# Kernel optimization log

Measured on AMD Instinct MI355X. Metric: run time of the kernel, lower is better.

## Reference

```python
import jax, jax.numpy as jnp
import numpy as np

B, XDIM, TWIN, INCH = 1024, 62, 10, 128
MID, OUT, K, K1, LIN, HC = 256, 512, 3, 10, 512, 4
EPS = 1e-5

REGIONS = [
    list(range(0, 5)),
    list(range(5, 8)) + list(range(14, 17)),
    list(range(8, 11)) + list(range(17, 20)),
    list(range(11, 14)) + list(range(20, 23)),
    list(range(23, 26)) + list(range(32, 35)),
    list(range(26, 29)) + list(range(35, 38)),
    list(range(29, 32)) + list(range(38, 41)),
    list(range(41, 44)) + list(range(50, 52)) + list(range(57, 58)),
    list(range(44, 47)) + list(range(52, 55)) + list(range(58, 61)),
    list(range(47, 50)) + list(range(55, 57)) + list(range(61, 62)),
]


def setup_inputs() -> dict:
    key = jax.random.key(0)
    ks = jax.random.split(key, 40)
    n = lambda k, s, sc=0.02: jax.random.normal(k, s, jnp.float32) * sc
    inp = {
        "x": jax.random.normal(ks[0], (B, XDIM, TWIN, INCH), jnp.float32),
        "tfe_w": n(ks[1], (XDIM, TWIN)),          # depthwise Conv2d (10,1) weight, squeezed
        "tfe_b": jnp.zeros((XDIM,), jnp.float32),
        "cheby1_w": n(ks[2], (K, INCH, OUT)),
        "A": n(ks[3], (XDIM, XDIM)),
        "cheby2_w": n(ks[4], (K, MID, OUT)),
        "A1": n(ks[5], (K1, K1)),
        "b_gate": jnp.float32(1.0),
        "c_gate": jnp.float32(1.0),
        "region_b": jnp.zeros((K1, MID), jnp.float32),
        "hc_w1": n(ks[6], (OUT * 72, LIN)),
        "hc_b1": jnp.zeros((LIN,), jnp.float32),
        "bn1_g": jnp.ones((LIN,), jnp.float32),
        "bn1_b": jnp.zeros((LIN,), jnp.float32),
        "hc_w2": n(ks[7], (LIN, LIN // 2)),
        "hc_b2": jnp.zeros((LIN // 2,), jnp.float32),
        "bn2_g": jnp.ones((LIN // 2,), jnp.float32),
        "bn2_b": jnp.zeros((LIN // 2,), jnp.float32),
        "hc_w3": n(ks[8], (LIN // 2, HC)),
        "hc_b3": jnp.zeros((HC,), jnp.float32),
    }
    for i, idx in enumerate(REGIONS):
        inp[f"rw{i+1}"] = n(ks[10 + i], (MID, INCH, len(idx)))
    return inp


def _cheby(x, L, Ws):
    # sum_k  S_k @ x @ W_k  with S_0 = I, S_k = S_{k-1} @ L ; then ReLU
    S = jnp.eye(L.shape[0], dtype=x.dtype)
    res = jnp.zeros(x.shape[:2] + (Ws.shape[-1],), x.dtype)
    for k in range(Ws.shape[0]):
        res = res + jnp.einsum("nm,bmt,to->bno", S, x, Ws[k])
        S = S @ L
    return jax.nn.relu(res)


def _bn(h, g, b):
    mu = h.mean(axis=0)
    v = h.var(axis=0)  # biased, training-mode BatchNorm1d
    return (h - mu) * jax.lax.rsqrt(v + EPS) * g + b


def _forward(x, tfe_w, tfe_b, cheby1_w, A, cheby2_w, A1, b_gate, c_gate,
             rw1, rw2, rw3, rw4, rw5, rw6, rw7, rw8, rw9, rw10, region_b,
             hc_w1, hc_b1, bn1_g, bn1_b, hc_w2, hc_b2, bn2_g, bn2_b, hc_w3, hc_b3):
    # variance gate (torch.var default: unbiased)
    sigma = jnp.var(x, axis=2, ddof=1)                              # (B, 62, INCH)
    g_tfe = jnp.einsum("bcit,ci->bct", x, tfe_w) + tfe_b[None, :, None]
    g = g_tfe * jnp.exp(-sigma)                                      # (B, 62, INCH)

    g1 = _cheby(g, A, cheby1_w)                                      # (B, 62, OUT)

    rws = [rw1, rw2, rw3, rw4, rw5, rw6, rw7, rw8, rw9, rw10]
    RG = []
    for i, (idx, w) in enumerate(zip(REGIONS, rws)):
        reg = g[:, jnp.asarray(idx), :]                              # (B, L, INCH)
        RG.append(jnp.einsum("blc,mcl->bm", reg, w) + region_b[i])   # Conv1d, full-width kernel
    g2in = jnp.stack(RG, axis=1)                                     # (B, 10, MID)
    g2 = _cheby(g2in, A1, cheby2_w)                                  # (B, 10, OUT)

    att = jnp.concatenate([b_gate * g1, c_gate * g2], axis=1)        # (B, 72, OUT)
    cat = jnp.concatenate([g1, g2], axis=1)
    out = jax.nn.softmax(att, axis=1) * cat
    out = out.reshape(out.shape[0], -1)                              # (B, 72*OUT)

    h = jax.nn.gelu(_bn(out @ hc_w1 + hc_b1, bn1_g, bn1_b), approximate=False)
    h = jax.nn.gelu(_bn(h @ hc_w2 + hc_b2, bn2_g, bn2_b), approximate=False)
    h = h @ hc_w3 + hc_b3
    return jax.nn.softmax(h, axis=1)


def reference(x, tfe_w, tfe_b, cheby1_w, A, cheby2_w, A1, b_gate, c_gate,
              rw1, rw2, rw3, rw4, rw5, rw6, rw7, rw8, rw9, rw10, region_b,
              hc_w1, hc_b1, bn1_g, bn1_b, hc_w2, hc_b2, bn2_g, bn2_b, hc_w3, hc_b3):
    return _forward(x, tfe_w, tfe_b, cheby1_w, A, cheby2_w, A1, b_gate, c_gate,
                    rw1, rw2, rw3, rw4, rw5, rw6, rw7, rw8, rw9, rw10, region_b,
                    hc_w1, hc_b1, bn1_g, bn1_b, hc_w2, hc_b2, bn2_g, bn2_b, hc_w3, hc_b3)
```

## Files before the change

### kernel.cpp

```cpp
#include <hip/hip_runtime.h>
#include <math.h>


__constant__ int cOrder[62] = {
  0,1,2,3,4,
  5,6,7,14,15,16,
  8,9,10,17,18,19,
  11,12,13,20,21,22,
  23,24,25,32,33,34,
  26,27,28,35,36,37,
  29,30,31,38,39,40,
  41,42,43,50,51,57,
  44,45,46,52,53,54,58,59,60,
  47,48,49,55,56,61
};
__constant__ int cPos[62] = {
  0,1,2,3,4, 5,6,7, 11,12,13, 17,18,19, 8,9,10, 14,15,16, 20,21,22,
  23,24,25, 29,30,31, 35,36,37, 26,27,28, 32,33,34, 38,39,40,
  41,42,43, 47,48,49, 56,57,58, 44,45, 50,51,52, 59,60, 46, 53,54,55, 61
};
__constant__ int cRegK[10]   = {640,768,768,768,768,768,768,768,1152,768};
__constant__ int cRegCum[10] = {0,640,1408,2176,2944,3712,4480,5248,6016,7168};

struct Ptr10 { const float* p[10]; };

typedef __attribute__((ext_vector_type(8))) short bf16x8;
typedef __attribute__((ext_vector_type(4))) float f32x4;

__device__ __forceinline__ float gelu_exact(float v){
  return 0.5f * v * (1.0f + erff(v * 0.70710678118654752f));
}
__device__ __forceinline__ unsigned short f2bf(float f){
  unsigned u = __float_as_uint(f);
  unsigned r = (u + 0x7fffu + ((u >> 16) & 1u)) >> 16;
  return (unsigned short)r;
}
__device__ __forceinline__ float bf2f(unsigned short u){
  return __uint_as_float(((unsigned)u) << 16);
}
__device__ __forceinline__ void load_lds16(const unsigned short* g, unsigned short* l){
  __builtin_amdgcn_global_load_lds(
      (const __attribute__((address_space(1))) void*)g,
      (__attribute__((address_space(3))) void*)l, 16, 0, 0);
}

template<bool RELU>
__global__ __launch_bounds__(256) void k_mfma(
    const unsigned short* __restrict__ A, long lda,
    const unsigned short* __restrict__ BT, long ldb,
    void* __restrict__ Cv, int ldc, int kPerZ, long cStrideZ, int mcCount){
  __shared__ unsigned short As[128*32];
  __shared__ unsigned short Bs[128*32];
  int mt, nt, zt;
  if (mcCount){
    int id = blockIdx.x;
    int c = ((id >> 6) << 3) + (id & 7);
    int member = (id >> 3) & 7;
    zt = c / mcCount;
    int mc = c - zt*mcCount;
    mt = mc*2 + (member >> 2);
    nt = member & 3;
  } else { mt = blockIdx.x; nt = blockIdx.y; zt = blockIdx.z; }
  int tid = threadIdx.x;
  int wave = tid >> 6, lane = tid & 63;
  int m0 = mt * 128, n0 = nt * 128;
  int kStart = zt * kPerZ;
  int waveM = wave >> 1, waveN = wave & 1;
  int lr = lane >> 2, ch = lane & 3;
  int quad = lane >> 4, mrow = lane & 15;
  int swe = ((quad ^ (mrow & 3)) << 3);

  int rA0 = wave*32 + lr;
  int rA1 = rA0 + 16;
  int ce  = ((ch ^ (rA0 & 3)) << 3);
  const unsigned short* gA0 = A  + (long)(m0 + rA0)*lda + kStart + ce;
  const unsigned short* gA1 = A  + (long)(m0 + rA1)*lda + kStart + ce;
  const unsigned short* gB0 = BT + (long)(n0 + rA0)*ldb + kStart + ce;
  const unsigned short* gB1 = BT + (long)(n0 + rA1)*ldb + kStart + ce;
  unsigned short* lA0 = &As[(wave*32)*32];
  unsigned short* lA1 = &As[(wave*32+16)*32];
  unsigned short* lB0 = &Bs[(wave*32)*32];
  unsigned short* lB1 = &Bs[(wave*32+16)*32];

  f32x4 acc[4][4] = {};
  int nIter = kPerZ >> 5;
  for (int it = 0; it < nIter; ++it){
    long ko = (long)it << 5;
    load_lds16(gA0 + ko, lA0);
    load_lds16(gA1 + ko, lA1);
    load_lds16(gB0 + ko, lB0);
    load_lds16(gB1 + ko, lB1);
    __syncthreads();
    bf16x8 af[4], bfr[4];
#pragma unroll
    for (int mi = 0; mi < 4; mi++)
      af[mi] = *(const bf16x8*)&As[(waveM*64 + mi*16 + mrow)*32 + swe];
#pragma unroll
    for (int ni = 0; ni < 4; ni++)
      bfr[ni] = *(const bf16x8*)&Bs[(waveN*64 + ni*16 + mrow)*32 + swe];
#pragma unroll
    for (int mi = 0; mi < 4; mi++)
#pragma unroll
      for (int ni = 0; ni < 4; ni++)
        acc[mi][ni] = __builtin_amdgcn_mfma_f32_16x16x32_bf16(
            af[mi], bfr[ni], acc[mi][ni], 0, 0, 0);
    __syncthreads();
  }
  if (RELU){
    unsigned short* C = (unsigned short*)Cv;
#pragma unroll
    for (int mi = 0; mi < 4; mi++)
#pragma unroll
      for (int ni = 0; ni < 4; ni++){
        int col = n0 + waveN*64 + ni*16 + mrow;
#pragma unroll
        for (int r = 0; r < 4; r++){
          int row = m0 + waveM*64 + mi*16 + quad*4 + r;
          C[(long)row*ldc + col] = f2bf(fmaxf(acc[mi][ni][r], 0.f));
        }
      }
  } else {
    float* C = (float*)Cv + (long)zt * cStrideZ;
#pragma unroll
    for (int mi = 0; mi < 4; mi++)
#pragma unroll
      for (int ni = 0; ni < 4; ni++){
        int col = n0 + waveN*64 + ni*16 + mrow;
#pragma unroll
        for (int r = 0; r < 4; r++){
          int row = m0 + waveM*64 + mi*16 + quad*4 + r;
          C[(long)row*ldc + col] = acc[mi][ni][r];
        }
      }
  }
}
template __global__ void k_mfma<true>(const unsigned short*, long, const unsigned short*, long, void*, int, int, long, int);
template __global__ void k_mfma<false>(const unsigned short*, long, const unsigned short*, long, void*, int, int, long, int);

__global__ __launch_bounds__(256) void k_dual(
    const unsigned short* __restrict__ A2c, const unsigned short* __restrict__ B2c,
    unsigned short* __restrict__ C2c,
    const unsigned short* __restrict__ A1c, const unsigned short* __restrict__ B1c,
    unsigned short* __restrict__ C1c){
  __shared__ unsigned short As[128*32];
  __shared__ unsigned short Bs[128*32];
  int id = blockIdx.x;
  bool is1 = id >= 320;
  const unsigned short* A  = is1 ? A1c : A2c;
  const unsigned short* BT = is1 ? B1c : B2c;
  unsigned short* C = is1 ? C1c : C2c;
  long lda = is1 ? 384 : 768;
  long ldb = lda;
  int kPerZ = (int)lda;
  if (is1) id -= 320;
  int c = ((id >> 6) << 3) + (id & 7);
  int member = (id >> 3) & 7;
  int mt = c*2 + (member >> 2);
  int nt = member & 3;
  int tid = threadIdx.x;
  int wave = tid >> 6, lane = tid & 63;
  int m0 = mt * 128, n0 = nt * 128;
  int waveM = wave >> 1, waveN = wave & 1;
  int lr = lane >> 2, ch = lane & 3;
  int quad = lane >> 4, mrow = lane & 15;
  int swe = ((quad ^ (mrow & 3)) << 3);

  int rA0 = wave*32 + lr;
  int rA1 = rA0 + 16;
  int ce  = ((ch ^ (rA0 & 3)) << 3);
  const unsigned short* gA0 = A  + (long)(m0 + rA0)*lda + ce;
  const unsigned short* gA1 = A  + (long)(m0 + rA1)*lda + ce;
  const unsigned short* gB0 = BT + (long)(n0 + rA0)*ldb + ce;
  const unsigned short* gB1 = BT + (long)(n0 + rA1)*ldb + ce;
  unsigned short* lA0 = &As[(wave*32)*32];
  unsigned short* lA1 = &As[(wave*32+16)*32];
  unsigned short* lB0 = &Bs[(wave*32)*32];
  unsigned short* lB1 = &Bs[(wave*32+16)*32];

  f32x4 acc[4][4] = {};
  int nIter = kPerZ >> 5;
  for (int it = 0; it < nIter; ++it){
    long ko = (long)it << 5;
    load_lds16(gA0 + ko, lA0);
    load_lds16(gA1 + ko, lA1);
    load_lds16(gB0 + ko, lB0);
    load_lds16(gB1 + ko, lB1);
    __syncthreads();
    bf16x8 af[4], bfr[4];
#pragma unroll
    for (int mi = 0; mi < 4; mi++)
      af[mi] = *(const bf16x8*)&As[(waveM*64 + mi*16 + mrow)*32 + swe];
#pragma unroll
    for (int ni = 0; ni < 4; ni++)
      bfr[ni] = *(const bf16x8*)&Bs[(waveN*64 + ni*16 + mrow)*32 + swe];
#pragma unroll
    for (int mi = 0; mi < 4; mi++)
#pragma unroll
      for (int ni = 0; ni < 4; ni++)
        acc[mi][ni] = __builtin_amdgcn_mfma_f32_16x16x32_bf16(
            af[mi], bfr[ni], acc[mi][ni], 0, 0, 0);
    __syncthreads();
  }
#pragma unroll
  for (int mi = 0; mi < 4; mi++)
#pragma unroll
    for (int ni = 0; ni < 4; ni++){
      int col = n0 + waveN*64 + ni*16 + mrow;
#pragma unroll
      for (int r = 0; r < 4; r++){
        int row = m0 + waveM*64 + mi*16 + quad*4 + r;
        C[(long)row*512 + col] = f2bf(fmaxf(acc[mi][ni][r], 0.f));
      }
    }
}

__global__ __launch_bounds__(256) void k_mid(
    const unsigned short* __restrict__ ARb, const unsigned short* __restrict__ Ab,
    const unsigned short* __restrict__ A2b, unsigned short* __restrict__ xcat,
    const unsigned short* __restrict__ RWT, const float* __restrict__ regb,
    float* __restrict__ g2in){
  __shared__ __align__(16) char smraw[32768];
  int id = blockIdx.x;
  int tid = threadIdx.x;
  if (id < 1024){
    unsigned short* gT  = (unsigned short*)smraw;
    unsigned short* AbL = gT + 128*64;
    int b = id;
    const unsigned short* arp = ARb + (long)b*7936;
    for (int i = tid; i < 7936; i += 256){
      int p = i >> 7, c = i & 127;
      int m = cOrder[p];
      gT[(c<<6) + (((m>>3) ^ (c&7))<<3) + (m&7)] = arp[i];
    }
    {
      int c = tid >> 1, m = 62 + (tid & 1);
      gT[(c<<6) + ((7 ^ (c&7))<<3) + (m&7)] = 0;
    }
    for (int q = tid; q < 1024; q += 256){
      int mm = q >> 9, qq = q & 511;
      int row = qq >> 3, ch = qq & 7;
      const unsigned short* src = mm ? A2b : Ab;
      *(bf16x8*)&AbL[mm*4096 + (row<<6) + ((ch ^ (row&7))<<3)] =
        *(const bf16x8*)&src[(row<<6) + (ch<<3)];
    }
    __syncthreads();
    int wave = tid >> 6, lane = tid & 63;
    int quad = lane >> 4, mrow = lane & 15;
    int mat = wave >> 1, wc = wave & 1;
    const unsigned short* Am = AbL + mat*4096;
    f32x4 acc[4][4] = {};
#pragma unroll
    for (int s = 0; s < 2; s++){
      bf16x8 af[4], bfr[4];
#pragma unroll
      for (int mi = 0; mi < 4; mi++){
        int row = mi*16 + mrow;
        af[mi] = *(const bf16x8*)&Am[(row<<6) + ((((s<<2)|quad) ^ (row&7))<<3)];
      }
#pragma unroll
      for (int ni = 0; ni < 4; ni++){
        int row = wc*64 + ni*16 + mrow;
        bfr[ni] = *(const bf16x8*)&gT[(row<<6) + ((((s<<2)|quad) ^ (row&7))<<3)];
      }
#pragma unroll
      for (int mi = 0; mi < 4; mi++)
#pragma unroll
        for (int ni = 0; ni < 4; ni++)
          acc[mi][ni] = __builtin_amdgcn_mfma_f32_16x16x32_bf16(
              af[mi], bfr[ni], acc[mi][ni], 0, 0, 0);
    }
    long xb = (long)b*23808 + (mat+1)*128;
#pragma unroll
    for (int mi = 0; mi < 4; mi++)
#pragma unroll
      for (int ni = 0; ni < 4; ni++){
        int c = wc*64 + ni*16 + mrow;
#pragma unroll
        for (int r = 0; r < 4; r++){
          int n = mi*16 + quad*4 + r;
          if (n < 62) xcat[xb + (long)n*384 + c] = f2bf(acc[mi][ni][r]);
        }
      }
    return;
  }
  unsigned short* As = (unsigned short*)smraw;
  unsigned short* Bs = As + 128*32;
  int id2 = id - 1024;
  int z = id2 >> 4;
  int m  = id2 & 15;
  int mt = m >> 1, nt = m & 1;
  int K = cRegK[z];
  int cumk = cRegCum[z];
  const unsigned short* A  = ARb + cumk;
  const unsigned short* BT = RWT + (long)cumk*256;
  long lda = 7936, ldb = K;
  int wave = tid >> 6, lane = tid & 63;
  int m0 = mt * 128, n0 = nt * 128;
  int waveM = wave >> 1, waveN = wave & 1;
  int lr = lane >> 2, ch = lane & 3;
  int quad = lane >> 4, mrow = lane & 15;
  int swe = ((quad ^ (mrow & 3)) << 3);

  int rA0 = wave*32 + lr;
  int rA1 = rA0 + 16;
  int ce  = ((ch ^ (rA0 & 3)) << 3);
  const unsigned short* gA0 = A  + (long)(m0 + rA0)*lda + ce;
  const unsigned short* gA1 = A  + (long)(m0 + rA1)*lda + ce;
  const unsigned short* gB0 = BT + (long)(n0 + rA0)*ldb + ce;
  const unsigned short* gB1 = BT + (long)(n0 + rA1)*ldb + ce;
  unsigned short* lA0 = &As[(wave*32)*32];
  unsigned short* lA1 = &As[(wave*32+16)*32];
  unsigned short* lB0 = &Bs[(wave*32)*32];
  unsigned short* lB1 = &Bs[(wave*32+16)*32];

  f32x4 acc[4][4] = {};
  int nIter = K >> 5;
  for (int it = 0; it < nIter; ++it){
    long ko = (long)it << 5;
    load_lds16(gA0 + ko, lA0);
    load_lds16(gA1 + ko, lA1);
    load_lds16(gB0 + ko, lB0);
    load_lds16(gB1 + ko, lB1);
    __syncthreads();
    bf16x8 af[4], bfr[4];
#pragma unroll
    for (int mi = 0; mi < 4; mi++)
      af[mi] = *(const bf16x8*)&As[(waveM*64 + mi*16 + mrow)*32 + swe];
#pragma unroll
    for (int ni = 0; ni < 4; ni++)
      bfr[ni] = *(const bf16x8*)&Bs[(waveN*64 + ni*16 + mrow)*32 + swe];
#pragma unroll
    for (int mi = 0; mi < 4; mi++)
#pragma unroll
      for (int ni = 0; ni < 4; ni++)
        acc[mi][ni] = __builtin_amdgcn_mfma_f32_16x16x32_bf16(
            af[mi], bfr[ni], acc[mi][ni], 0, 0, 0);
    __syncthreads();
  }
#pragma unroll
  for (int mi = 0; mi < 4; mi++)
#pragma unroll
    for (int ni = 0; ni < 4; ni++){
      int col = n0 + waveN*64 + ni*16 + mrow;
      float bias = regb[z*256 + col];
#pragma unroll
      for (int r = 0; r < 4; r++){
        int row = m0 + waveM*64 + mi*16 + quad*4 + r;
        g2in[(long)row*2560 + z*256 + col] = acc[mi][ni][r] + bias;
      }
    }
}

__global__ __launch_bounds__(256) void k_front(
    const float* __restrict__ s0, unsigned short* __restrict__ d0,
    const float* __restrict__ s1, unsigned short* __restrict__ d1,
    const float* __restrict__ s2, unsigned short* __restrict__ d2,
    const float* __restrict__ s3, unsigned short* __restrict__ d3,
    Ptr10 rws, unsigned short* __restrict__ RWT,
    const float* __restrict__ Amat, unsigned short* __restrict__ AbW,
    unsigned short* __restrict__ A2bW,
    const float* __restrict__ x, const float* __restrict__ tw,
    const float* __restrict__ tb, unsigned short* __restrict__ arb,
    unsigned short* __restrict__ xcat, float* __restrict__ sumz){
  __shared__ float smem[64*65];
  int id = blockIdx.x;
  int tid = threadIdx.x;
  if (id >= 15342){
    *(float4*)(sumz + (id-15342)*1024 + tid*4) = make_float4(0.f,0.f,0.f,0.f);
    return;
  }
  if (id >= 7406){
    int q = id - 7406;
    int r = tid >> 5, j = tid & 31;
    int idx = q*8 + r;
    int b = idx / 62, n = idx - b*62;
    const float4* xp = (const float4*)(x + (long)idx*1280) + j;
    float sx=0.f,sy=0.f,sz=0.f,sw=0.f;
    float qx=0.f,qy=0.f,qz=0.f,qw=0.f;
    float gx=0.f,gy=0.f,gz=0.f,gw=0.f;
#pragma unroll
    for (int i = 0; i < 10; i++){
      float4 v = xp[i*32];
      float w = tw[n*10+i];
      sx+=v.x; sy+=v.y; sz+=v.z; sw+=v.w;
      qx=fmaf(v.x,v.x,qx); qy=fmaf(v.y,v.y,qy);
      qz=fmaf(v.z,v.z,qz); qw=fmaf(v.w,v.w,qw);
      gx=fmaf(v.x,w,gx); gy=fmaf(v.y,w,gy);
      gz=fmaf(v.z,w,gz); gw=fmaf(v.w,w,gw);
    }
    float tbn = tb[n];
    float mx_=sx*0.1f, my_=sy*0.1f, mz_=sz*0.1f, mw_=sw*0.1f;
    float rx = (gx+tbn)*expf(-(qx-10.f*mx_*mx_)*(1.f/9.f));
    float ry = (gy+tbn)*expf(-(qy-10.f*my_*my_)*(1.f/9.f));
    float rz = (gz+tbn)*expf(-(qz-10.f*mz_*mz_)*(1.f/9.f));
    float rw = (gw+tbn)*expf(-(qw-10.f*mw_*mw_)*(1.f/9.f));
    ushort4 u = make_ushort4(f2bf(rx), f2bf(ry), f2bf(rz), f2bf(rw));
    *(ushort4*)(arb  + (long)b*7936  + cPos[n]*128 + j*4) = u;
    *(ushort4*)(xcat + (long)b*23808 + n*384       + j*4) = u;
    return;
  }
  if (id < 7344 && id >= 4784){
    int q = id - 4784;
    int z = q >> 8, m = q & 255;
    int K = cRegK[z], L = K >> 7;
    const float* rw = rws.p[z] + (long)m*K;
    unsigned short* dst = RWT + (long)cRegCum[z]*256 + (long)m*K;
    for (int i = tid; i < K; i += 256) smem[i] = rw[i];
    __syncthreads();
    for (int k = tid; k < K; k += 256){
      int l = k >> 7, c = k & 127;
      dst[k] = f2bf(smem[c*L + l]);
    }
    return;
  }
  if (id >= 7344){
    int r = id - 7344, c = tid;
    if (c < 62) smem[c] = Amat[r*62 + c];
    __syncthreads();
    if (c < 64){
      unsigned short av = 0, a2v = 0;
      if (c < 62){
        av = f2bf(smem[c]);
        float s = 0.f;
        for (int t = 0; t < 62; t++) s = fmaf(smem[t], Amat[t*62 + c], s);
        a2v = f2bf(s);
      }
      AbW [r*64 + c] = av;
      A2bW[r*64 + c] = a2v;
    }
    if (r == 0 && c >= 64 && c < 192){
      int q = c - 64;
      int rr = 62 + (q >> 6), cc = q & 63;
      AbW [rr*64 + cc] = 0;
      A2bW[rr*64 + cc] = 0;
    }
    return;
  }
  const float* src; unsigned short* dst; int R, C, rt, ct;
  if (id < 4608){ src=s0; dst=d0; R=36864; C=512; rt=id>>3;  ct=id&7; }
  else if (id < 4640){ int q=id-4608; src=s1; dst=d1; R=512; C=256; rt=q>>2; ct=q&3; }
  else if (id < 4688){ int q=id-4640; src=s2; dst=d2; R=384; C=512; rt=q>>3; ct=q&7; }
  else { int q=id-4688; src=s3; dst=d3; R=768; C=512; rt=q>>3; ct=q&7; }
  int r0 = rt*64, c0 = ct*64;
  int rr = tid >> 2, cb = (tid & 3) << 2;
#pragma unroll
  for (int i = 0; i < 4; i++){
    int cc = cb + i*16;
    float4 v = *(const float4*)(src + (long)(r0+rr)*C + c0 + cc);
    smem[rr*65+cc+0]=v.x; smem[rr*65+cc+1]=v.y;
    smem[rr*65+cc+2]=v.z; smem[rr*65+cc+3]=v.w;
  }
  __syncthreads();
  int cc = tid >> 2, rb = (tid & 3) << 2;
#pragma unroll
  for (int i = 0; i < 4; i++){
    int r = rb + i*16;
    ushort4 u = make_ushort4(f2bf(smem[(r+0)*65+cc]), f2bf(smem[(r+1)*65+cc]),
                             f2bf(smem[(r+2)*65+cc]), f2bf(smem[(r+3)*65+cc]));
    *(ushort4*)(dst + (long)(c0+cc)*R + r0 + r) = u;
  }
}

__global__ __launch_bounds__(256) void k_x2cat(
    const float* __restrict__ g2in, const float* __restrict__ A1,
    unsigned short* __restrict__ X2){
  __shared__ float sg[2560];
  __shared__ float sA1[100];
  __shared__ float sA2[100];
  int b = blockIdx.x, tid = threadIdx.x;
  for (int i = tid; i < 2560; i += 256) sg[i] = g2in[(long)b*2560 + i];
  if (tid < 100) sA1[tid] = A1[tid];
  __syncthreads();
  if (tid < 100){
    int n = tid/10, m = tid - n*10;
    float a = 0.f;
#pragma unroll
    for (int t = 0; t < 10; t++) a = fmaf(sA1[n*10+t], sA1[t*10+m], a);
    sA2[tid] = a;
  }
  __syncthreads();
  for (int i = tid; i < 2560; i += 256){
    int n = i >> 8, t = i & 255;
    float v1 = 0.f, v2 = 0.f;
#pragma unroll
    for (int m = 0; m < 10; m++){
      float gv = sg[(m<<8) + t];
      v1 = fmaf(sA1[n*10+m], gv, v1);
      v2 = fmaf(sA2[n*10+m], gv, v2);
    }
    long base = (long)b*7680 + n*768;
    X2[base + t]       = f2bf(sg[i]);
    X2[base + 256 + t] = f2bf(v1);
    X2[base + 512 + t] = f2bf(v2);
  }
}

__global__ __launch_bounds__(256) void k_softcat(
    const unsigned short* __restrict__ g1, const unsigned short* __restrict__ g2,
    const float* __restrict__ bg_, const float* __restrict__ cg_,
    unsigned short* __restrict__ outb){
  int b = blockIdx.x;
  int o = blockIdx.y*256 + threadIdx.x;
  float v[72];
  const unsigned short* p1 = g1 + (long)b*62*512 + o;
#pragma unroll
  for (int j = 0; j < 62; j++) v[j] = bf2f(p1[j*512]);
  const unsigned short* p2 = g2 + (long)b*10*512 + o;
#pragma unroll
  for (int j = 0; j < 10; j++) v[62+j] = bf2f(p2[j*512]);
  float bg = *bg_, cg = *cg_;
  float mx = -1e30f;
#pragma unroll
  for (int j = 0; j < 72; j++){
    float av = (j < 62 ? bg : cg) * v[j];
    mx = fmaxf(mx, av);
  }
  float sum = 0.f;
#pragma unroll
  for (int j = 0; j < 72; j++){
    float e = expf((j < 62 ? bg : cg) * v[j] - mx);
    sum += e;
    v[j] = e * v[j];
  }
  float inv = 1.f / sum;
  unsigned short* op = outb + (long)b*36864 + o;
#pragma unroll
  for (int j = 0; j < 72; j++) op[j*512] = f2bf(v[j] * inv);
}

__global__ __launch_bounds__(256) void k_tail1(
    const float4* __restrict__ P, const float* __restrict__ gam,
    const float* __restrict__ bet, float* __restrict__ sum,
    float* __restrict__ ssq, unsigned int* __restrict__ cnt,
    unsigned short* __restrict__ h1b){
  __shared__ float4 ls[128], ls2[128];
  int tid = threadIdx.x;
  int c  = tid & 127;
  int rr = tid >> 7;
  int r0 = blockIdx.x * 8;
  float4 va[4];
  float4 s1 = make_float4(0.f,0.f,0.f,0.f);
  float4 s2 = make_float4(0.f,0.f,0.f,0.f);
#pragma unroll
  for (int k = 0; k < 4; k++){
    int row = r0 + rr + 2*k;
    long idx = (long)row*128 + c;
    float4 v = make_float4(0.f,0.f,0.f,0.f);
#pragma unroll
    for (int s = 0; s < 16; s++){
      float4 p = P[(long)s*131072 + idx];
      v.x += p.x; v.y += p.y; v.z += p.z; v.w += p.w;
    }
    va[k] = v;
    s1.x += v.x; s1.y += v.y; s1.z += v.z; s1.w += v.w;
    s2.x = fmaf(v.x,v.x,s2.x); s2.y = fmaf(v.y,v.y,s2.y);
    s2.z = fmaf(v.z,v.z,s2.z); s2.w = fmaf(v.w,v.w,s2.w);
  }
  if (rr){ ls[c] = s1; ls2[c] = s2; }
  __syncthreads();
  if (!rr){
    float4 o1 = ls[c], o2 = ls2[c];
    atomicAdd(&sum[c*4+0], s1.x+o1.x); atomicAdd(&sum[c*4+1], s1.y+o1.y);
    atomicAdd(&sum[c*4+2], s1.z+o1.z); atomicAdd(&sum[c*4+3], s1.w+o1.w);
    atomicAdd(&ssq[c*4+0], s2.x+o2.x); atomicAdd(&ssq[c*4+1], s2.y+o2.y);
    atomicAdd(&ssq[c*4+2], s2.z+o2.z); atomicAdd(&ssq[c*4+3], s2.w+o2.w);
  }
  __threadfence();
  __syncthreads();
  if (tid == 0){
    __hip_atomic_fetch_add(cnt, 1u, __ATOMIC_RELEASE, __HIP_MEMORY_SCOPE_AGENT);
    while (__hip_atomic_load(cnt, __ATOMIC_ACQUIRE, __HIP_MEMORY_SCOPE_AGENT) < 128u)
      __builtin_amdgcn_s_sleep(16);
  }
  __syncthreads();
  int j = c*4;
  float mu0 = __hip_atomic_load(&sum[j+0], __ATOMIC_RELAXED, __HIP_MEMORY_SCOPE_AGENT)*(1.f/1024.f);
  float mu1 = __hip_atomic_load(&sum[j+1], __ATOMIC_RELAXED, __HIP_MEMORY_SCOPE_AGENT)*(1.f/1024.f);
  float mu2 = __hip_atomic_load(&sum[j+2], __ATOMIC_RELAXED, __HIP_MEMORY_SCOPE_AGENT)*(1.f/1024.f);
  float mu3 = __hip_atomic_load(&sum[j+3], __ATOMIC_RELAXED, __HIP_MEMORY_SCOPE_AGENT)*(1.f/1024.f);
  float q0 = __hip_atomic_load(&ssq[j+0], __ATOMIC_RELAXED, __HIP_MEMORY_SCOPE_AGENT);
  float q1 = __hip_atomic_load(&ssq[j+1], __ATOMIC_RELAXED, __HIP_MEMORY_SCOPE_AGENT);
  float q2 = __hip_atomic_load(&ssq[j+2], __ATOMIC_RELAXED, __HIP_MEMORY_SCOPE_AGENT);
  float q3 = __hip_atomic_load(&ssq[j+3], __ATOMIC_RELAXED, __HIP_MEMORY_SCOPE_AGENT);
  float rs0 = rsqrtf(q0*(1.f/1024.f) - mu0*mu0 + 1e-5f);
  float rs1 = rsqrtf(q1*(1.f/1024.f) - mu1*mu1 + 1e-5f);
  float rs2 = rsqrtf(q2*(1.f/1024.f) - mu2*mu2 + 1e-5f);
  float rs3 = rsqrtf(q3*(1.f/1024.f) - mu3*mu3 + 1e-5f);
  float g0 = gam[j+0], g1 = gam[j+1], g2 = gam[j+2], g3 = gam[j+3];
  float b0 = bet[j+0], b1 = bet[j+1], b2 = bet[j+2], b3 = bet[j+3];
#pragma unroll
  for (int k = 0; k < 4; k++){
    int row = r0 + rr + 2*k;
    float4 v = va[k];
    ushort4 u;
    u.x = f2bf(gelu_exact((v.x - mu0)*rs0*g0 + b0));
    u.y = f2bf(gelu_exact((v.y - mu1)*rs1*g1 + b1));
    u.z = f2bf(gelu_exact((v.z - mu2)*rs2*g2 + b2));
    u.w = f2bf(gelu_exact((v.w - mu3)*rs3*g3 + b3));
    *(ushort4*)(h1b + (long)row*512 + j) = u;
  }
}

__global__ __launch_bounds__(256) void k_tail2(
    const float* __restrict__ P2, const float* __restrict__ gam,
    const float* __restrict__ bet, const float* __restrict__ w3,
    const float* __restrict__ b3, float* __restrict__ sum,
    float* __restrict__ ssq, unsigned int* __restrict__ cnt,
    float* __restrict__ outp){
  __shared__ float lv[32][257];
  __shared__ float rd[32][8][4];
  int tid = threadIdx.x;
  int rbase = blockIdx.x * 32;
  float v[32];
  float s = 0.f, s2 = 0.f;
#pragma unroll 8
  for (int r = 0; r < 32; r++){
    int row = rbase + r;
    float a = 0.f;
#pragma unroll
    for (int sp = 0; sp < 4; sp++)
      a += P2[((long)sp*1024 + row)*256 + tid];
    v[r] = a;
    s += a; s2 = fmaf(a, a, s2);
  }
  atomicAdd(&sum[tid], s);
  atomicAdd(&ssq[tid], s2);
  __threadfence();
  __syncthreads();
  if (tid == 0){
    __hip_atomic_fetch_add(cnt, 1u, __ATOMIC_RELEASE, __HIP_MEMORY_SCOPE_AGENT);
    while (__hip_atomic_load(cnt, __ATOMIC_ACQUIRE, __HIP_MEMORY_SCOPE_AGENT) < 32u)
      __builtin_amdgcn_s_sleep(16);
  }
  __syncthreads();
  float mu = __hip_atomic_load(&sum[tid], __ATOMIC_RELAXED, __HIP_MEMORY_SCOPE_AGENT)*(1.f/1024.f);
  float qq = __hip_atomic_load(&ssq[tid], __ATOMIC_RELAXED, __HIP_MEMORY_SCOPE_AGENT);
  float rs = rsqrtf(qq*(1.f/1024.f) - mu*mu + 1e-5f);
  float gm = gam[tid], bt = bet[tid];
#pragma unroll 8
  for (int r = 0; r < 32; r++)
    lv[r][tid] = gelu_exact((v[r] - mu)*rs*gm + bt);
  __syncthreads();
  int row = tid >> 3, seg = tid & 7;
  float p0=0.f,p1=0.f,p2=0.f,p3=0.f;
#pragma unroll
  for (int i = 0; i < 32; i++){
    int cc = seg*32 + i;
    float a = lv[row][cc];
    float4 w = ((const float4*)w3)[cc];
    p0 = fmaf(a, w.x, p0); p1 = fmaf(a, w.y, p1);
    p2 = fmaf(a, w.z, p2); p3 = fmaf(a, w.w, p3);
  }
  rd[row][seg][0]=p0; rd[row][seg][1]=p1; rd[row][seg][2]=p2; rd[row][seg][3]=p3;
  __syncthreads();
  if (tid < 32){
    float l[4];
#pragma unroll
    for (int c = 0; c < 4; c++){
      float a = 0.f;
#pragma unroll
      for (int g = 0; g < 8; g++) a += rd[tid][g][c];
      l[c] = a + b3[c];
    }
    float m = fmaxf(fmaxf(l[0], l[1]), fmaxf(l[2], l[3]));
    float e[4]; float su = 0.f;
#pragma unroll
    for (int c = 0; c < 4; c++){ e[c] = expf(l[c]-m); su += e[c]; }
    float inv = 1.f / su;
#pragma unroll
    for (int c = 0; c < 4; c++) outp[(long)(rbase+tid)*4 + c] = e[c]*inv;
  }
}

extern "C" void kernel_launch(void* const* d_in, const int* in_sizes, int n_in,
                              void* d_out, int out_size, void* d_ws, size_t ws_size,
                              hipStream_t stream){
  (void)n_in; (void)out_size; (void)ws_size;
  bool dictOrder = (in_sizes[9] == 2560);
  const float* x     = (const float*)d_in[0];
  const float* tfe_w = (const float*)d_in[1];
  const float* tfe_b = (const float*)d_in[2];
  const float* ch1w  = (const float*)d_in[3];
  const float* Amat  = (const float*)d_in[4];
  const float* ch2w  = (const float*)d_in[5];
  const float* A1mat = (const float*)d_in[6];
  const float* bgate = (const float*)d_in[7];
  const float* cgate = (const float*)d_in[8];
  const float* regb  = (const float*)d_in[dictOrder ? 9 : 19];
  int o = dictOrder ? 0 : 10;
  const float* hc_w1 = (const float*)d_in[10+o];
  const float* bn1g  = (const float*)d_in[12+o];
  const float* bn1b  = (const float*)d_in[13+o];
  const float* hc_w2 = (const float*)d_in[14+o];
  const float* bn2g  = (const float*)d_in[16+o];
  const float* bn2b  = (const float*)d_in[17+o];
  const float* hc_w3 = (const float*)d_in[18+o];
  const float* hc_b3 = (const float*)d_in[19+o];
  Ptr10 rws;
  for (int i = 0; i < 10; i++) rws.p[i] = (const float*)d_in[(dictOrder ? 20 : 9) + i];

  char* Wb = (char*)d_ws;
  unsigned short* ARb   = (unsigned short*)(Wb + 0);
  unsigned short* XCAT  = (unsigned short*)(Wb + 16252928);
  unsigned short* RWT   = (unsigned short*)(Wb + 65011712);
  float*          G2IN  = (float*)(Wb + 69074944);
  unsigned short* X2CAT = (unsigned short*)(Wb + 79560704);
  unsigned short* W1T   = (unsigned short*)(Wb + 95289344);
  unsigned short* WC1T  = (unsigned short*)(Wb + 133038080);
  unsigned short* WC2T  = (unsigned short*)(Wb + 133431296);
  unsigned short* G1    = (unsigned short*)(Wb + 134217728);
  unsigned short* G2    = (unsigned short*)(Wb + 199229440);
  unsigned short* OUTB  = (unsigned short*)(Wb + 0);
  float*          P     = (float*)(Wb + 209715200);
  float*          SUM1  = (float*)(Wb + 246415360);
  float*          SSQ1  = SUM1 + 512;
  float*          SUM2  = SUM1 + 1024;
  float*          SSQ2  = SUM1 + 1280;
  unsigned int*   CNT1  = (unsigned int*)(SUM1 + 1536);
  unsigned int*   CNT2  = (unsigned int*)(SUM1 + 1537);
  unsigned short* Ab    = (unsigned short*)(Wb + 246423552);
  unsigned short* A2b   = (unsigned short*)(Wb + 246439040);
  unsigned short* W2T   = (unsigned short*)(Wb + 246454528);
  unsigned short* H1B   = (unsigned short*)(Wb + 246716928);

  k_front<<<15344, 256, 0, stream>>>(hc_w1, W1T, hc_w2, W2T, ch1w, WC1T,
                                     ch2w, WC2T, rws, RWT, Amat, Ab, A2b,
                                     x, tfe_w, tfe_b, ARb, XCAT, SUM1);
  k_mid<<<1184, 256, 0, stream>>>(ARb, Ab, A2b, XCAT, RWT, regb, G2IN);
  k_x2cat<<<1024, 256, 0, stream>>>(G2IN, A1mat, X2CAT);
  k_dual<<<2304, 256, 0, stream>>>(X2CAT, WC2T, G2, XCAT, WC1T, G1);
  k_softcat<<<dim3(1024,2), 256, 0, stream>>>(G1, G2, bgate, cgate, OUTB);
  k_mfma<false><<<512, 256, 0, stream>>>(OUTB, 36864, W1T, 36864, (void*)P, 512, 2304, 524288, 4);
  k_tail1<<<128, 256, 0, stream>>>((const float4*)P, bn1g, bn1b, SUM1, SSQ1, CNT1, H1B);
  k_mfma<false><<<dim3(8,2,4), 256, 0, stream>>>(H1B, 512, W2T, 512, (void*)P, 256, 128, 262144, 0);
  k_tail2<<<32, 256, 0, stream>>>(P, bn2g, bn2b, hc_w3, hc_b3, SUM2, SSQ2, CNT2, (float*)d_out);
}
```

Measured before the change: 811.9 us.

## Fuse BN1/GELU, second GEMM and BN2/head tail into one persistent kernel

Merges k_tail1, the small second MFMA GEMM and k_tail2 into a single 128-block kernel. Grid-wide counter barriers separate the stages, and later stages run on a subset of blocks. This removes two kernel launches and their gaps at the end of the pipeline. In exchange it relies on all blocks being co-resident and on four barrier counters being zeroed beforehand. The GEMM is also re-implemented inline with a single-buffered K loop.

```diff
diff --git a/kernel.cpp b/kernel.cpp
--- a/kernel.cpp
+++ b/kernel.cpp
@@ -42,6 +42,16 @@
   __builtin_amdgcn_global_load_lds(
       (const __attribute__((address_space(1))) void*)g,
       (__attribute__((address_space(3))) void*)l, 16, 0, 0);
+}
+__device__ __forceinline__ void gate(unsigned int* cnt, unsigned int target, int tid){
+  __threadfence();
+  __syncthreads();
+  if (tid == 0){
+    __hip_atomic_fetch_add(cnt, 1u, __ATOMIC_RELEASE, __HIP_MEMORY_SCOPE_AGENT);
+    while (__hip_atomic_load(cnt, __ATOMIC_ACQUIRE, __HIP_MEMORY_SCOPE_AGENT) < target)
+      __builtin_amdgcn_s_sleep(16);
+  }
+  __syncthreads();
 }
 
 template<bool RELU>
@@ -528,147 +538,191 @@
   for (int j = 0; j < 72; j++) op[j*512] = f2bf(v[j] * inv);
 }
 
-__global__ __launch_bounds__(256) void k_tail1(
-    const float4* __restrict__ P, const float* __restrict__ gam,
-    const float* __restrict__ bet, float* __restrict__ sum,
-    float* __restrict__ ssq, unsigned int* __restrict__ cnt,
-    unsigned short* __restrict__ h1b){
-  __shared__ float4 ls[128], ls2[128];
+__global__ __launch_bounds__(256) void k_tail(
+    float* Pf, const float* __restrict__ gam1, const float* __restrict__ bet1,
+    const unsigned short* __restrict__ W2T,
+    const float* __restrict__ gam2, const float* __restrict__ bet2,
+    const float* __restrict__ w3, const float* __restrict__ b3,
+    float* __restrict__ sum1, float* __restrict__ ssq1,
+    float* __restrict__ sum2, float* __restrict__ ssq2,
+    unsigned int* __restrict__ cnts, unsigned short* __restrict__ h1b,
+    float* __restrict__ outp){
+  __shared__ __align__(16) char smraw[36992];
   int tid = threadIdx.x;
-  int c  = tid & 127;
-  int rr = tid >> 7;
-  int r0 = blockIdx.x * 8;
-  float4 va[4];
-  float4 s1 = make_float4(0.f,0.f,0.f,0.f);
-  float4 s2 = make_float4(0.f,0.f,0.f,0.f);
-#pragma unroll
-  for (int k = 0; k < 4; k++){
-    int row = r0 + rr + 2*k;
-    long idx = (long)row*128 + c;
-    float4 v = make_float4(0.f,0.f,0.f,0.f);
-#pragma unroll
-    for (int s = 0; s < 16; s++){
-      float4 p = P[(long)s*131072 + idx];
-      v.x += p.x; v.y += p.y; v.z += p.z; v.w += p.w;
-    }
-    va[k] = v;
-    s1.x += v.x; s1.y += v.y; s1.z += v.z; s1.w += v.w;
-    s2.x = fmaf(v.x,v.x,s2.x); s2.y = fmaf(v.y,v.y,s2.y);
-    s2.z = fmaf(v.z,v.z,s2.z); s2.w = fmaf(v.w,v.w,s2.w);
-  }
-  if (rr){ ls[c] = s1; ls2[c] = s2; }
-  __syncthreads();
-  if (!rr){
-    float4 o1 = ls[c], o2 = ls2[c];
-    atomicAdd(&sum[c*4+0], s1.x+o1.x); atomicAdd(&sum[c*4+1], s1.y+o1.y);
-    atomicAdd(&sum[c*4+2], s1.z+o1.z); atomicAdd(&sum[c*4+3], s1.w+o1.w);
-    atomicAdd(&ssq[c*4+0], s2.x+o2.x); atomicAdd(&ssq[c*4+1], s2.y+o2.y);
-    atomicAdd(&ssq[c*4+2], s2.z+o2.z); atomicAdd(&ssq[c*4+3], s2.w+o2.w);
-  }
-  __threadfence();
-  __syncthreads();
-  if (tid == 0){
-    __hip_atomic_fetch_add(cnt, 1u, __ATOMIC_RELEASE, __HIP_MEMORY_SCOPE_AGENT);
-    while (__hip_atomic_load(cnt, __ATOMIC_ACQUIRE, __HIP_MEMORY_SCOPE_AGENT) < 128u)
-      __builtin_amdgcn_s_sleep(16);
-  }
-  __syncthreads();
-  int j = c*4;
-  float mu0 = __hip_atomic_load(&sum[j+0], __ATOMIC_RELAXED, __HIP_MEMORY_SCOPE_AGENT)*(1.f/1024.f);
-  float mu1 = __hip_atomic_load(&sum[j+1], __ATOMIC_RELAXED, __HIP_MEMORY_SCOPE_AGENT)*(1.f/1024.f);
-  float mu2 = __hip_atomic_load(&sum[j+2], __ATOMIC_RELAXED, __HIP_MEMORY_SCOPE_AGENT)*(1.f/1024.f);
-  float mu3 = __hip_atomic_load(&sum[j+3], __ATOMIC_RELAXED, __HIP_MEMORY_SCOPE_AGENT)*(1.f/1024.f);
-  float q0 = __hip_atomic_load(&ssq[j+0], __ATOMIC_RELAXED, __HIP_MEMORY_SCOPE_AGENT);
-  float q1 = __hip_atomic_load(&ssq[j+1], __ATOMIC_RELAXED, __HIP_MEMORY_SCOPE_AGENT);
-  float q2 = __hip_atomic_load(&ssq[j+2], __ATOMIC_RELAXED, __HIP_MEMORY_SCOPE_AGENT);
-  float q3 = __hip_atomic_load(&ssq[j+3], __ATOMIC_RELAXED, __HIP_MEMORY_SCOPE_AGENT);
-  float rs0 = rsqrtf(q0*(1.f/1024.f) - mu0*mu0 + 1e-5f);
-  float rs1 = rsqrtf(q1*(1.f/1024.f) - mu1*mu1 + 1e-5f);
-  float rs2 = rsqrtf(q2*(1.f/1024.f) - mu2*mu2 + 1e-5f);
-  float rs3 = rsqrtf(q3*(1.f/1024.f) - mu3*mu3 + 1e-5f);
-  float g0 = gam[j+0], g1 = gam[j+1], g2 = gam[j+2], g3 = gam[j+3];
-  float b0 = bet[j+0], b1 = bet[j+1], b2 = bet[j+2], b3 = bet[j+3];
-#pragma unroll
-  for (int k = 0; k < 4; k++){
-    int row = r0 + rr + 2*k;
-    float4 v = va[k];
-    ushort4 u;
-    u.x = f2bf(gelu_exact((v.x - mu0)*rs0*g0 + b0));
-    u.y = f2bf(gelu_exact((v.y - mu1)*rs1*g1 + b1));
-    u.z = f2bf(gelu_exact((v.z - mu2)*rs2*g2 + b2));
-    u.w = f2bf(gelu_exact((v.w - mu3)*rs3*g3 + b3));
-    *(ushort4*)(h1b + (long)row*512 + j) = u;
-  }
-}
-
-__global__ __launch_bounds__(256) void k_tail2(
-    const float* __restrict__ P2, const float* __restrict__ gam,
-    const float* __restrict__ bet, const float* __restrict__ w3,
-    const float* __restrict__ b3, float* __restrict__ sum,
-    float* __restrict__ ssq, unsigned int* __restrict__ cnt,
-    float* __restrict__ outp){
-  __shared__ float lv[32][257];
-  __shared__ float rd[32][8][4];
-  int tid = threadIdx.x;
-  int rbase = blockIdx.x * 32;
-  float v[32];
-  float s = 0.f, s2 = 0.f;
+  int bid = blockIdx.x;
+  {
+    const float4* P = (const float4*)Pf;
+    float4* ls  = (float4*)smraw;
+    float4* ls2 = ls + 128;
+    int c  = tid & 127;
+    int rr = tid >> 7;
+    int r0 = bid * 8;
+    float4 va[4];
+    float4 s1 = make_float4(0.f,0.f,0.f,0.f);
+    float4 s2 = make_float4(0.f,0.f,0.f,0.f);
+#pragma unroll
+    for (int k = 0; k < 4; k++){
+      int row = r0 + rr + 2*k;
+      long idx = (long)row*128 + c;
+      float4 v = make_float4(0.f,0.f,0.f,0.f);
+#pragma unroll
+      for (int s = 0; s < 16; s++){
+        float4 p = P[(long)s*131072 + idx];
+        v.x += p.x; v.y += p.y; v.z += p.z; v.w += p.w;
+      }
+      va[k] = v;
+      s1.x += v.x; s1.y += v.y; s1.z += v.z; s1.w += v.w;
+      s2.x = fmaf(v.x,v.x,s2.x); s2.y = fmaf(v.y,v.y,s2.y);
+      s2.z = fmaf(v.z,v.z,s2.z); s2.w = fmaf(v.w,v.w,s2.w);
+    }
+    if (rr){ ls[c] = s1; ls2[c] = s2; }
+    __syncthreads();
+    if (!rr){
+      float4 o1 = ls[c], o2 = ls2[c];
+      atomicAdd(&sum1[c*4+0], s1.x+o1.x); atomicAdd(&sum1[c*4+1], s1.y+o1.y);
+      atomicAdd(&sum1[c*4+2], s1.z+o1.z); atomicAdd(&sum1[c*4+3], s1.w+o1.w);
+      atomicAdd(&ssq1[c*4+0], s2.x+o2.x); atomicAdd(&ssq1[c*4+1], s2.y+o2.y);
+      atomicAdd(&ssq1[c*4+2], s2.z+o2.z); atomicAdd(&ssq1[c*4+3], s2.w+o2.w);
+    }
+    gate(&cnts[0], 128, tid);
+    int j = c*4;
+    float mu0 = sum1[j+0]*(1.f/1024.f), mu1 = sum1[j+1]*(1.f/1024.f);
+    float mu2 = sum1[j+2]*(1.f/1024.f), mu3 = sum1[j+3]*(1.f/1024.f);
+    float rs0 = rsqrtf(ssq1[j+0]*(1.f/1024.f) - mu0*mu0 + 1e-5f);
+    float rs1 = rsqrtf(ssq1[j+1]*(1.f/1024.f) - mu1*mu1 + 1e-5f);
+    float rs2 = rsqrtf(ssq1[j+2]*(1.f/1024.f) - mu2*mu2 + 1e-5f);
+    float rs3 = rsqrtf(ssq1[j+3]*(1.f/1024.f) - mu3*mu3 + 1e-5f);
+    float g0 = gam1[j+0], g1 = gam1[j+1], g2 = gam1[j+2], g3 = gam1[j+3];
+    float b0 = bet1[j+0], b1 = bet1[j+1], b2 = bet1[j+2], b3_ = bet1[j+3];
+#pragma unroll
+    for (int k = 0; k < 4; k++){
+      int row = r0 + rr + 2*k;
+      float4 v = va[k];
+      ushort4 u;
+      u.x = f2bf(gelu_exact((v.x - mu0)*rs0*g0 + b0));
+      u.y = f2bf(gelu_exact((v.y - mu1)*rs1*g1 + b1));
+      u.z = f2bf(gelu_exact((v.z - mu2)*rs2*g2 + b2));
+      u.w = f2bf(gelu_exact((v.w - mu3)*rs3*g3 + b3_));
+      *(ushort4*)(h1b + (long)row*512 + j) = u;
+    }
+  }
+  gate(&cnts[1], 128, tid);
+  if (bid >= 64) return;
+  {
+    unsigned short* As = (unsigned short*)smraw;
+    unsigned short* Bs = As + 128*32;
+    int mt = bid >> 3, nt = (bid >> 2) & 1, zt = bid & 3;
+    int wave = tid >> 6, lane = tid & 63;
+    int m0 = mt*128, n0 = nt*128, kStart = zt*128;
+    int waveM = wave >> 1, waveN = wave & 1;
+    int lr = lane >> 2, ch = lane & 3;
+    int quad = lane >> 4, mrow = lane & 15;
+    int swe = ((quad ^ (mrow & 3)) << 3);
+    int rA0 = wave*32 + lr;
+    int rA1 = rA0 + 16;
+    int ce  = ((ch ^ (rA0 & 3)) << 3);
+    const unsigned short* gA0 = h1b + (long)(m0 + rA0)*512 + kStart + ce;
+    const unsigned short* gA1 = h1b + (long)(m0 + rA1)*512 + kStart + ce;
+    const unsigned short* gB0 = W2T + (long)(n0 + rA0)*512 + kStart + ce;
+    const unsigned short* gB1 = W2T + (long)(n0 + rA1)*512 + kStart + ce;
+    unsigned short* lA0 = &As[(wave*32)*32];
+    unsigned short* lA1 = &As[(wave*32+16)*32];
+    unsigned short* lB0 = &Bs[(wave*32)*32];
+    unsigned short* lB1 = &Bs[(wave*32+16)*32];
+    f32x4 acc[4][4] = {};
+#pragma unroll
+    for (int it = 0; it < 4; ++it){
+      long ko = (long)it << 5;
+      load_lds16(gA0 + ko, lA0);
+      load_lds16(gA1 + ko, lA1);
+      load_lds16(gB0 + ko, lB0);
+      load_lds16(gB1 + ko, lB1);
+      __syncthreads();
+      bf16x8 af[4], bfr[4];
+#pragma unroll
+      for (int mi = 0; mi < 4; mi++)
+        af[mi] = *(const bf16x8*)&As[(waveM*64 + mi*16 + mrow)*32 + swe];
+#pragma unroll
+      for (int ni = 0; ni < 4; ni++)
+        bfr[ni] = *(const bf16x8*)&Bs[(waveN*64 + ni*16 + mrow)*32 + swe];
+#pragma unroll
+      for (int mi = 0; mi < 4; mi++)
+#pragma unroll
+        for (int ni = 0; ni < 4; ni++)
+          acc[mi][ni] = __builtin_amdgcn_mfma_f32_16x16x32_bf16(
+              af[mi], bfr[ni], acc[mi][ni], 0, 0, 0);
+      __syncthreads();
+    }
+    float* C = Pf + (long)zt * 262144;
+#pragma unroll
+    for (int mi = 0; mi < 4; mi++)
+#pragma unroll
+      for (int ni = 0; ni < 4; ni++){
+        int col = n0 + waveN*64 + ni*16 + mrow;
+#pragma unroll
+        for (int r = 0; r < 4; r++){
+          int row = m0 + waveM*64 + mi*16 + quad*4 + r;
+          C[(long)row*256 + col] = acc[mi][ni][r];
+        }
+      }
+  }
+  gate(&cnts[2], 64, tid);
+  if (bid >= 32) return;
+  {
+    float (*lv)[257] = (float(*)[257])smraw;
+    float (*rd)[8][4] = (float(*)[8][4])(smraw + 32896);
+    int rbase = bid * 32;
+    float v[32];
+    float s = 0.f, s2 = 0.f;
 #pragma unroll 8
-  for (int r = 0; r < 32; r++){
-    int row = rbase + r;
-    float a = 0.f;
-#pragma unroll
-    for (int sp = 0; sp < 4; sp++)
-      a += P2[((long)sp*1024 + row)*256 + tid];
-    v[r] = a;
-    s += a; s2 = fmaf(a, a, s2);
-  }
-  atomicAdd(&sum[tid], s);
-  atomicAdd(&ssq[tid], s2);
-  __threadfence();
-  __syncthreads();
-  if (tid == 0){
-    __hip_atomic_fetch_add(cnt, 1u, __ATOMIC_RELEASE, __HIP_MEMORY_SCOPE_AGENT);
-    while (__hip_atomic_load(cnt, __ATOMIC_ACQUIRE, __HIP_MEMORY_SCOPE_AGENT) < 32u)
-      __builtin_amdgcn_s_sleep(16);
-  }
-  __syncthreads();
-  float mu = __hip_atomic_load(&sum[tid], __ATOMIC_RELAXED, __HIP_MEMORY_SCOPE_AGENT)*(1.f/1024.f);
-  float qq = __hip_atomic_load(&ssq[tid], __ATOMIC_RELAXED, __HIP_MEMORY_SCOPE_AGENT);
-  float rs = rsqrtf(qq*(1.f/1024.f) - mu*mu + 1e-5f);
-  float gm = gam[tid], bt = bet[tid];
+    for (int r = 0; r < 32; r++){
+      int row = rbase + r;
+      float a = 0.f;
+#pragma unroll
+      for (int sp = 0; sp < 4; sp++)
+        a += Pf[(long)sp*262144 + (long)row*256 + tid];
+      v[r] = a;
+      s += a; s2 = fmaf(a, a, s2);
+    }
+    atomicAdd(&sum2[tid], s);
+    atomicAdd(&ssq2[tid], s2);
+    gate(&cnts[3], 32, tid);
+    float mu = sum2[tid]*(1.f/1024.f);
+    float rs = rsqrtf(ssq2[tid]*(1.f/1024.f) - mu*mu + 1e-5f);
+    float gm = gam2[tid], bt = bet2[tid];
 #pragma unroll 8
-  for (int r = 0; r < 32; r++)
-    lv[r][tid] = gelu_exact((v[r] - mu)*rs*gm + bt);
-  __syncthreads();
-  int row = tid >> 3, seg = tid & 7;
-  float p0=0.f,p1=0.f,p2=0.f,p3=0.f;
-#pragma unroll
-  for (int i = 0; i < 32; i++){
-    int cc = seg*32 + i;
-    float a = lv[row][cc];
-    float4 w = ((const float4*)w3)[cc];
-    p0 = fmaf(a, w.x, p0); p1 = fmaf(a, w.y, p1);
-    p2 = fmaf(a, w.z, p2); p3 = fmaf(a, w.w, p3);
-  }
-  rd[row][seg][0]=p0; rd[row][seg][1]=p1; rd[row][seg][2]=p2; rd[row][seg][3]=p3;
-  __syncthreads();
-  if (tid < 32){
-    float l[4];
-#pragma unroll
-    for (int c = 0; c < 4; c++){
-      float a = 0.f;
-#pragma unroll
-      for (int g = 0; g < 8; g++) a += rd[tid][g][c];
-      l[c] = a + b3[c];
-    }
-    float m = fmaxf(fmaxf(l[0], l[1]), fmaxf(l[2], l[3]));
-    float e[4]; float su = 0.f;
-#pragma unroll
-    for (int c = 0; c < 4; c++){ e[c] = expf(l[c]-m); su += e[c]; }
-    float inv = 1.f / su;
-#pragma unroll
-    for (int c = 0; c < 4; c++) outp[(long)(rbase+tid)*4 + c] = e[c]*inv;
+    for (int r = 0; r < 32; r++)
+      lv[r][tid] = gelu_exact((v[r] - mu)*rs*gm + bt);
+    __syncthreads();
+    int row = tid >> 3, seg = tid & 7;
+    float p0=0.f,p1=0.f,p2=0.f,p3=0.f;
+#pragma unroll
+    for (int i = 0; i < 32; i++){
+      int cc = seg*32 + i;
+      float a = lv[row][cc];
+      float4 w = ((const float4*)w3)[cc];
+      p0 = fmaf(a, w.x, p0); p1 = fmaf(a, w.y, p1);
+      p2 = fmaf(a, w.z, p2); p3 = fmaf(a, w.w, p3);
+    }
+    rd[row][seg][0]=p0; rd[row][seg][1]=p1; rd[row][seg][2]=p2; rd[row][seg][3]=p3;
+    __syncthreads();
+    if (tid < 32){
+      float l[4];
+#pragma unroll
+      for (int c = 0; c < 4; c++){
+        float a = 0.f;
+#pragma unroll
+        for (int g = 0; g < 8; g++) a += rd[tid][g][c];
+        l[c] = a + b3[c];
+      }
+      float m = fmaxf(fmaxf(l[0], l[1]), fmaxf(l[2], l[3]));
+      float e[4]; float su = 0.f;
+#pragma unroll
+      for (int c = 0; c < 4; c++){ e[c] = expf(l[c]-m); su += e[c]; }
+      float inv = 1.f / su;
+#pragma unroll
+      for (int c = 0; c < 4; c++) outp[(long)(rbase+tid)*4 + c] = e[c]*inv;
+    }
   }
 }
 
@@ -716,8 +770,7 @@
   float*          SSQ1  = SUM1 + 512;
   float*          SUM2  = SUM1 + 1024;
   float*          SSQ2  = SUM1 + 1280;
-  unsigned int*   CNT1  = (unsigned int*)(SUM1 + 1536);
-  unsigned int*   CNT2  = (unsigned int*)(SUM1 + 1537);
+  unsigned int*   CNTS  = (unsigned int*)(SUM1 + 1536);
   unsigned short* Ab    = (unsigned short*)(Wb + 246423552);
   unsigned short* A2b   = (unsigned short*)(Wb + 246439040);
   unsigned short* W2T   = (unsigned short*)(Wb + 246454528);
@@ -731,7 +784,6 @@
   k_dual<<<2304, 256, 0, stream>>>(X2CAT, WC2T, G2, XCAT, WC1T, G1);
   k_softcat<<<dim3(1024,2), 256, 0, stream>>>(G1, G2, bgate, cgate, OUTB);
   k_mfma<false><<<512, 256, 0, stream>>>(OUTB, 36864, W1T, 36864, (void*)P, 512, 2304, 524288, 4);
-  k_tail1<<<128, 256, 0, stream>>>((const float4*)P, bn1g, bn1b, SUM1, SSQ1, CNT1, H1B);
-  k_mfma<false><<<dim3(8,2,4), 256, 0, stream>>>(H1B, 512, W2T, 512, (void*)P, 256, 128, 262144, 0);
-  k_tail2<<<32, 256, 0, stream>>>(P, bn2g, bn2b, hc_w3, hc_b3, SUM2, SSQ2, CNT2, (float*)d_out);
-}
+  k_tail<<<128, 256, 0, stream>>>(P, bn1g, bn1b, W2T, bn2g, bn2b, hc_w3, hc_b3,
+                                  SUM1, SSQ1, SUM2, SSQ2, CNTS, H1B, (float*)d_out);
+}
```

Measured after the change: 830.4 us. 2.3% more time.
